# Optimization experiments

Hardware: AMD Instinct MI355X
Metric: run time of the kernel (lower is better)

Reference implementation:

```python
import jax, jax.numpy as jnp
import numpy as np

B = 256        # trees per batch
DEPTH = 10     # complete binary tree depth -> 2^10 - 1 = 1023 internal nodes
N = 2**DEPTH - 1
IN = 128       # input_size
H = 128        # hidden_size
C = 5          # num_classes


def setup_inputs() -> dict:
    key = jax.random.key(0)
    ks = jax.random.split(key, 13)
    gdim = IN + 2 * H  # concat(x, h_left, h_right)
    inp = {"x": jax.random.normal(ks[0], (B, N, IN), jnp.float32)}
    names = ["i", "fl", "fr", "o", "u"]
    for j, nm in enumerate(names):
        inp[f"W_{nm}"] = 0.05 * jax.random.normal(ks[1 + 2 * j], (H, gdim), jnp.float32)
        inp[f"b_{nm}"] = 0.05 * jax.random.normal(ks[2 + 2 * j], (H,), jnp.float32)
    inp["W_cls"] = 0.05 * jax.random.normal(ks[11], (C, H), jnp.float32)
    inp["b_cls"] = 0.05 * jax.random.normal(ks[12], (C,), jnp.float32)
    return inp


def reference(x, W_i, b_i, W_fl, b_fl, W_fr, b_fr, W_o, b_o, W_u, b_u, W_cls, b_cls):
    # Level-order complete binary tree: node k has children 2k+1, 2k+2.
    # Bottom-up sweep; below the deepest internal level all children are
    # empty nodes with h = c = 0 (matches the original base case).
    Bb = x.shape[0]
    h = jnp.zeros((Bb, 2 ** DEPTH, H), x.dtype)
    c = jnp.zeros_like(h)
    for d in range(DEPTH - 1, -1, -1):  # fixed, small structural loop
        n = 2 ** d
        start = n - 1  # level-order offset of level d
        xs = x[:, start:start + n]            # [B, n, IN]
        hl, hr = h[:, 0::2], h[:, 1::2]       # children of node j are 2j, 2j+1 (level-local)
        cl, cr = c[:, 0::2], c[:, 1::2]
        comb = jnp.concatenate([xs, hl, hr], axis=-1)  # [B, n, IN+2H]
        lin = lambda W, b: jnp.einsum('bng,og->bno', comb, W) + b
        i = jax.nn.sigmoid(lin(W_i, b_i))
        fl = jax.nn.sigmoid(lin(W_fl, b_fl))
        fr = jax.nn.sigmoid(lin(W_fr, b_fr))
        o = jax.nn.sigmoid(lin(W_o, b_o))
        u = jnp.tanh(lin(W_u, b_u))
        c = i * u + fl * cl + fr * cr
        h = o * jnp.tanh(c)
    root_h = h[:, 0]                          # [B, H]
    logits = root_h @ W_cls.T + b_cls         # [B, C]
    return logits
```

## Files before the change

### kernel.cpp

```cpp
#include <hip/hip_runtime.h>
#include <hip/hip_bf16.h>
#include <stdint.h>


#define BATCH 256
#define NTOT 1023
#define HDIM 128
#define NCLS 5
#define GDIM 384

typedef __bf16 bf16x8 __attribute__((ext_vector_type(8)));
typedef float f32x4 __attribute__((ext_vector_type(4)));

__device__ __forceinline__ float sigmoid_f(float v) { return 1.f / (1.f + __expf(-v)); }
__device__ __forceinline__ float tanh_f(float v) { return 1.f - 2.f / (1.f + __expf(2.f * v)); }

__global__ __launch_bounds__(256) void pack_w(
    const float* __restrict__ W0, const float* __restrict__ W1, const float* __restrict__ W2,
    const float* __restrict__ W3, const float* __restrict__ W4, __bf16* __restrict__ PW)
{
  int t = blockIdx.x * 256 + threadIdx.x;
  int lane = t & 63;
  int chunk = t >> 6;
  int ks = chunk % 12;
  int jf = (chunk / 12) & 7;
  int g = chunk / 96;
  const float* W = (g == 0) ? W0 : (g == 1) ? W1 : (g == 2) ? W2 : (g == 3) ? W3 : W4;
  const float* s = W + (size_t)(jf * 16 + (lane & 15)) * GDIM + ks * 32 + (lane >> 4) * 8;
  float4 v0 = *(const float4*)s;
  float4 v1 = *(const float4*)(s + 4);
  bf16x8 w;
  w[0] = (__bf16)v0.x; w[1] = (__bf16)v0.y; w[2] = (__bf16)v0.z; w[3] = (__bf16)v0.w;
  w[4] = (__bf16)v1.x; w[5] = (__bf16)v1.y; w[6] = (__bf16)v1.z; w[7] = (__bf16)v1.w;
  *(bf16x8*)(PW + (size_t)t * 8) = w;
}

#define LDS_TOT 75264
#define Q_OFF   50176
#define CSTR    132

template<int NMF, bool LEAF, bool LAST>
__device__ __forceinline__ void fused_level(
    const float* __restrict__ xp,
    const __bf16* __restrict__ PW,
    const float* __restrict__ bv0, const float* __restrict__ bv1,
    const float* __restrict__ bv2, const float* __restrict__ bv3,
    const float* __restrict__ bv4,
    const unsigned char* prev_h, const float* prev_c,
    unsigned char* cur_h, float* cur_c,
    __bf16* __restrict__ gh, float* __restrict__ gc,
    int nvalid)
{
  const int tid = threadIdx.x;
  const int w = tid >> 6;
  const int l = tid & 63;
  const int l15 = l & 15;
  const int quad = l >> 4;
  const int q8 = quad * 8;
  constexpr int NACC = LEAF ? 3 : 5;
  constexpr int NKT = LEAF ? 4 : 12;

  const bf16x8* PB = (const bf16x8*)PW;

  bf16x8 bb[2][NACC];
  bf16x8 xb[2][NMF];

  auto loadB = [&](int buf, int ks) {
#pragma unroll
    for (int q = 0; q < NACC; ++q) {
      const int g = LEAF ? (q ? q + 2 : 0) : q;
      bb[buf][q] = PB[((size_t)(g * 8 + w) * 12 + ks) * 64 + l];
    }
  };
  auto loadX = [&](int buf, int kx) {
#pragma unroll
    for (int mf = 0; mf < NMF; ++mf) {
      const float* xr = xp + (size_t)(mf * 16 + l15) * HDIM + q8 + kx * 32;
      float4 v0 = *(const float4*)xr;
      float4 v1 = *(const float4*)(xr + 4);
      bf16x8 t;
      t[0] = (__bf16)v0.x; t[1] = (__bf16)v0.y; t[2] = (__bf16)v0.z; t[3] = (__bf16)v0.w;
      t[4] = (__bf16)v1.x; t[5] = (__bf16)v1.y; t[6] = (__bf16)v1.z; t[7] = (__bf16)v1.w;
      xb[buf][mf] = t;
    }
  };

  loadB(0, 0);
  loadX(0, 0);
  loadB(1, 1);
  loadX(1, 1);

  f32x4 acc[NMF][NACC];
#pragma unroll
  for (int mf = 0; mf < NMF; ++mf)
#pragma unroll
    for (int q = 0; q < NACC; ++q)
      acc[mf][q] = (f32x4){0.f, 0.f, 0.f, 0.f};

#pragma unroll
  for (int ks = 0; ks < NKT; ++ks) {
    const int cb = ks & 1;
    bf16x8 a[NMF];
#pragma unroll
    for (int mf = 0; mf < NMF; ++mf) {
      if (LEAF || ks < 4) {
        a[mf] = xb[cb][mf];
      } else {
        const int o = (ks < 8) ? 0 : 1;
        const int col2 = ((ks - (o ? 8 : 4)) * 32 + q8) * 2;
        const int nn = 2 * (mf * 16 + l15) + o;
        a[mf] = *(const bf16x8*)(prev_h + nn * 256 + (col2 ^ ((nn & 7) << 4)));
      }
    }
#pragma unroll
    for (int q = 0; q < NACC; ++q)
#pragma unroll
      for (int mf = 0; mf < NMF; ++mf)
        acc[mf][q] = __builtin_amdgcn_mfma_f32_16x16x32_bf16(a[mf], bb[cb][q], acc[mf][q], 0, 0, 0);
    if (ks + 2 < NKT) loadB(cb, ks + 2);
    if (ks + 2 < 4)   loadX(cb, ks + 2);
  }

  const int je = w * 16 + l15;
  const float b0 = bv0[je], b3v = bv3[je], b4v = bv4[je];
#pragma unroll
  for (int mf = 0; mf < NMF; ++mf) {
#pragma unroll
    for (int r = 0; r < 4; ++r) {
      const int me = mf * 16 + quad * 4 + r;
      if (me < nvalid) {
        float gi = sigmoid_f(acc[mf][0][r] + b0);
        float go = sigmoid_f(acc[mf][LEAF ? 1 : 3][r] + b3v);
        float gu = tanh_f(acc[mf][LEAF ? 2 : 4][r] + b4v);
        float cv = gi * gu;
        if constexpr (!LEAF) {
          float gl = sigmoid_f(acc[mf][1][r] + bv1[je]);
          float gr = sigmoid_f(acc[mf][2][r] + bv2[je]);
          cv += gl * prev_c[(2 * me) * CSTR + je] + gr * prev_c[(2 * me + 1) * CSTR + je];
        }
        float hv = go * tanh_f(cv);
        if constexpr (LAST) {
          gc[(size_t)me * HDIM + je] = cv;
          gh[(size_t)me * HDIM + je] = (__bf16)hv;
        } else {
          cur_c[me * CSTR + je] = cv;
          *(__bf16*)(cur_h + me * 256 + ((je * 2) ^ ((me & 7) << 4))) = (__bf16)hv;
        }
      }
    }
  }
}

__global__ __launch_bounds__(512, 4) void fused_top(
    const float* __restrict__ x, const __bf16* __restrict__ PW,
    const float* __restrict__ bv0, const float* __restrict__ bv1,
    const float* __restrict__ bv2, const float* __restrict__ bv3,
    const float* __restrict__ bv4,
    __bf16* __restrict__ h6, float* __restrict__ c6)
{
  __shared__ unsigned char lds[LDS_TOT];
  const int b = blockIdx.x >> 3;
  const int s = blockIdx.x & 7;
  unsigned char* Ph = lds;
  float* Pc = (float*)(lds + 16384);
  unsigned char* Qh = lds + Q_OFF;
  float* Qc = (float*)(lds + Q_OFF + 8192);
  const size_t xb = (size_t)b * NTOT;

  fused_level<4, true, false>(x + (xb + 511 + s * 64) * HDIM, PW,
      bv0, bv1, bv2, bv3, bv4, nullptr, nullptr, Ph, Pc, nullptr, nullptr, 64);
  __syncthreads();
  fused_level<2, false, false>(x + (xb + 255 + s * 32) * HDIM, PW,
      bv0, bv1, bv2, bv3, bv4, Ph, Pc, Qh, Qc, nullptr, nullptr, 32);
  __syncthreads();
  fused_level<1, false, false>(x + (xb + 127 + s * 16) * HDIM, PW,
      bv0, bv1, bv2, bv3, bv4, Qh, Qc, Ph, Pc, nullptr, nullptr, 16);
  __syncthreads();
  fused_level<1, false, true>(x + (xb + 63 + s * 8) * HDIM, PW,
      bv0, bv1, bv2, bv3, bv4, Ph, Pc, nullptr, nullptr,
      h6 + ((size_t)b * 64 + s * 8) * HDIM, c6 + ((size_t)b * 64 + s * 8) * HDIM, 8);
}

__global__ __launch_bounds__(512, 4) void tail_kernel(
    const float* __restrict__ x, const __bf16* __restrict__ PW,
    const float* __restrict__ bv0, const float* __restrict__ bv1,
    const float* __restrict__ bv2, const float* __restrict__ bv3,
    const float* __restrict__ bv4,
    const float* __restrict__ Wcls, const float* __restrict__ bcls,
    const __bf16* __restrict__ h6, const float* __restrict__ c6,
    float* __restrict__ out)
{
  __shared__ unsigned char lds[LDS_TOT];
  const int b = blockIdx.x;
  const int tid = threadIdx.x;
  unsigned char* Ph = lds;
  float* Pc = (float*)(lds + 16384);
  unsigned char* Qh = lds + Q_OFF;
  float* Qc = (float*)(lds + Q_OFF + 8192);

  {
    const __bf16* hs = h6 + (size_t)b * 64 * HDIM;
#pragma unroll
    for (int it = 0; it < 2; ++it) {
      int idx = it * 512 + tid;
      int node = idx >> 4, i8 = idx & 15;
      bf16x8 v = *(const bf16x8*)(hs + node * HDIM + i8 * 8);
      *(bf16x8*)(Ph + node * 256 + ((i8 * 16) ^ ((node & 7) << 4))) = v;
    }
    const float* cs = c6 + (size_t)b * 64 * HDIM;
#pragma unroll
    for (int it = 0; it < 4; ++it) {
      int idx = it * 512 + tid;
      int node = idx >> 5, seg = idx & 31;
      float4 v = *(const float4*)(cs + node * HDIM + seg * 4);
      *(float4*)(Pc + node * CSTR + seg * 4) = v;
    }
  }
  __syncthreads();

  const size_t xb = (size_t)b * NTOT;
  fused_level<2, false, false>(x + (xb + 31) * HDIM, PW,
      bv0, bv1, bv2, bv3, bv4, Ph, Pc, Qh, Qc, nullptr, nullptr, 32);
  __syncthreads();
  fused_level<1, false, false>(x + (xb + 15) * HDIM, PW,
      bv0, bv1, bv2, bv3, bv4, Qh, Qc, Ph, Pc, nullptr, nullptr, 16);
  __syncthreads();
  fused_level<1, false, false>(x + (xb + 7) * HDIM, PW,
      bv0, bv1, bv2, bv3, bv4, Ph, Pc, Qh, Qc, nullptr, nullptr, 8);
  __syncthreads();
  fused_level<1, false, false>(x + (xb + 3) * HDIM, PW,
      bv0, bv1, bv2, bv3, bv4, Qh, Qc, Ph, Pc, nullptr, nullptr, 4);
  __syncthreads();
  fused_level<1, false, false>(x + (xb + 1) * HDIM, PW,
      bv0, bv1, bv2, bv3, bv4, Ph, Pc, Qh, Qc, nullptr, nullptr, 2);
  __syncthreads();
  fused_level<1, false, false>(x + (xb + 0) * HDIM, PW,
      bv0, bv1, bv2, bv3, bv4, Qh, Qc, Ph, Pc, nullptr, nullptr, 1);
  __syncthreads();

  if (tid < NCLS) {
    float sacc = bcls[tid];
    for (int k = 0; k < HDIM; ++k)
      sacc += (float)(*(const __bf16*)(Ph + k * 2)) * Wcls[tid * HDIM + k];
    out[(size_t)b * NCLS + tid] = sacc;
  }
}

extern "C" void kernel_launch(void* const* d_in, const int* in_sizes, int n_in,
                              void* d_out, int out_size, void* d_ws, size_t ws_size,
                              hipStream_t stream) {
  const float* x  = (const float*)d_in[0];
  const float* W[5]  = {(const float*)d_in[1], (const float*)d_in[3], (const float*)d_in[5],
                        (const float*)d_in[7], (const float*)d_in[9]};
  const float* bv[5] = {(const float*)d_in[2], (const float*)d_in[4], (const float*)d_in[6],
                        (const float*)d_in[8], (const float*)d_in[10]};
  const float* Wcls = (const float*)d_in[11];
  const float* bcls = (const float*)d_in[12];

  uint8_t* ws = (uint8_t*)d_ws;
  __bf16* hb1 = (__bf16*)(ws + 33554432);
  float*  cb1 = (float*)(ws + 117440512);
  __bf16* PW  = (__bf16*)(ws + 150994944);

  pack_w<<<120, 256, 0, stream>>>(W[0], W[1], W[2], W[3], W[4], PW);

  fused_top<<<BATCH * 8, 512, 0, stream>>>(
      x, PW, bv[0], bv[1], bv[2], bv[3], bv[4], hb1, cb1);

  tail_kernel<<<BATCH, 512, 0, stream>>>(
      x, PW, bv[0], bv[1], bv[2], bv[3], bv[4],
      Wcls, bcls, hb1, cb1, (float*)d_out);
}
```

Baseline: 544.6 us.

## Drop register double-buffering in fused_level and split leaf level into two halves

```diff
diff --git a/kernel.cpp b/kernel.cpp
--- a/kernel.cpp
+++ b/kernel.cpp
@@ -59,66 +59,62 @@
   const int q8 = quad * 8;
   constexpr int NACC = LEAF ? 3 : 5;
   constexpr int NKT = LEAF ? 4 : 12;
-
   const bf16x8* PB = (const bf16x8*)PW;
 
-  bf16x8 bb[2][NACC];
-  bf16x8 xb[2][NMF];
-
-  auto loadB = [&](int buf, int ks) {
+  f32x4 acc[NMF][NACC];
+#pragma unroll
+  for (int mf = 0; mf < NMF; ++mf)
+#pragma unroll
+    for (int q = 0; q < NACC; ++q)
+      acc[mf][q] = (f32x4){0.f, 0.f, 0.f, 0.f};
+
+#pragma unroll
+  for (int ks = 0; ks < NKT; ++ks) {
+    bf16x8 bq[NACC];
 #pragma unroll
     for (int q = 0; q < NACC; ++q) {
       const int g = LEAF ? (q ? q + 2 : 0) : q;
-      bb[buf][q] = PB[((size_t)(g * 8 + w) * 12 + ks) * 64 + l];
-    }
-  };
-  auto loadX = [&](int buf, int kx) {
-#pragma unroll
-    for (int mf = 0; mf < NMF; ++mf) {
-      const float* xr = xp + (size_t)(mf * 16 + l15) * HDIM + q8 + kx * 32;
-      float4 v0 = *(const float4*)xr;
-      float4 v1 = *(const float4*)(xr + 4);
-      bf16x8 t;
-      t[0] = (__bf16)v0.x; t[1] = (__bf16)v0.y; t[2] = (__bf16)v0.z; t[3] = (__bf16)v0.w;
-      t[4] = (__bf16)v1.x; t[5] = (__bf16)v1.y; t[6] = (__bf16)v1.z; t[7] = (__bf16)v1.w;
-      xb[buf][mf] = t;
-    }
-  };
-
-  loadB(0, 0);
-  loadX(0, 0);
-  loadB(1, 1);
-  loadX(1, 1);
-
-  f32x4 acc[NMF][NACC];
-#pragma unroll
-  for (int mf = 0; mf < NMF; ++mf)
-#pragma unroll
-    for (int q = 0; q < NACC; ++q)
-      acc[mf][q] = (f32x4){0.f, 0.f, 0.f, 0.f};
-
-#pragma unroll
-  for (int ks = 0; ks < NKT; ++ks) {
-    const int cb = ks & 1;
-    bf16x8 a[NMF];
-#pragma unroll
-    for (int mf = 0; mf < NMF; ++mf) {
-      if (LEAF || ks < 4) {
-        a[mf] = xb[cb][mf];
-      } else {
-        const int o = (ks < 8) ? 0 : 1;
-        const int col2 = ((ks - (o ? 8 : 4)) * 32 + q8) * 2;
-        const int nn = 2 * (mf * 16 + l15) + o;
-        a[mf] = *(const bf16x8*)(prev_h + nn * 256 + (col2 ^ ((nn & 7) << 4)));
-      }
-    }
-#pragma unroll
-    for (int q = 0; q < NACC; ++q)
-#pragma unroll
-      for (int mf = 0; mf < NMF; ++mf)
-        acc[mf][q] = __builtin_amdgcn_mfma_f32_16x16x32_bf16(a[mf], bb[cb][q], acc[mf][q], 0, 0, 0);
-    if (ks + 2 < NKT) loadB(cb, ks + 2);
-    if (ks + 2 < 4)   loadX(cb, ks + 2);
+      bq[q] = PB[((size_t)(g * 8 + w) * 12 + ks) * 64 + l];
+    }
+    bf16x8 a0, a1;
+    if (LEAF || ks < 4) {
+      const int kx = LEAF ? ks : ks;
+      {
+        const float* xr = xp + (size_t)l15 * HDIM + q8 + kx * 32;
+        float4 v0 = *(const float4*)xr;
+        float4 v1 = *(const float4*)(xr + 4);
+        bf16x8 t;
+        t[0] = (__bf16)v0.x; t[1] = (__bf16)v0.y; t[2] = (__bf16)v0.z; t[3] = (__bf16)v0.w;
+        t[4] = (__bf16)v1.x; t[5] = (__bf16)v1.y; t[6] = (__bf16)v1.z; t[7] = (__bf16)v1.w;
+        a0 = t;
+      }
+      if constexpr (NMF == 2) {
+        const float* xr = xp + (size_t)(16 + l15) * HDIM + q8 + kx * 32;
+        float4 v0 = *(const float4*)xr;
+        float4 v1 = *(const float4*)(xr + 4);
+        bf16x8 t;
+        t[0] = (__bf16)v0.x; t[1] = (__bf16)v0.y; t[2] = (__bf16)v0.z; t[3] = (__bf16)v0.w;
+        t[4] = (__bf16)v1.x; t[5] = (__bf16)v1.y; t[6] = (__bf16)v1.z; t[7] = (__bf16)v1.w;
+        a1 = t;
+      }
+    } else {
+      const int o = (ks < 8) ? 0 : 1;
+      const int col2 = ((ks - (o ? 8 : 4)) * 32 + q8) * 2;
+      {
+        const int nn = 2 * l15 + o;
+        a0 = *(const bf16x8*)(prev_h + nn * 256 + (col2 ^ ((nn & 7) << 4)));
+      }
+      if constexpr (NMF == 2) {
+        const int nn = 2 * (16 + l15) + o;
+        a1 = *(const bf16x8*)(prev_h + nn * 256 + (col2 ^ ((nn & 7) << 4)));
+      }
+    }
+#pragma unroll
+    for (int q = 0; q < NACC; ++q) {
+      acc[0][q] = __builtin_amdgcn_mfma_f32_16x16x32_bf16(a0, bq[q], acc[0][q], 0, 0, 0);
+      if constexpr (NMF == 2)
+        acc[1][q] = __builtin_amdgcn_mfma_f32_16x16x32_bf16(a1, bq[q], acc[1][q], 0, 0, 0);
+    }
   }
 
   const int je = w * 16 + l15;
@@ -167,8 +163,11 @@
   float* Qc = (float*)(lds + Q_OFF + 8192);
   const size_t xb = (size_t)b * NTOT;
 
-  fused_level<4, true, false>(x + (xb + 511 + s * 64) * HDIM, PW,
-      bv0, bv1, bv2, bv3, bv4, nullptr, nullptr, Ph, Pc, nullptr, nullptr, 64);
+  fused_level<2, true, false>(x + (xb + 511 + s * 64) * HDIM, PW,
+      bv0, bv1, bv2, bv3, bv4, nullptr, nullptr, Ph, Pc, nullptr, nullptr, 32);
+  fused_level<2, true, false>(x + (xb + 511 + s * 64 + 32) * HDIM, PW,
+      bv0, bv1, bv2, bv3, bv4, nullptr, nullptr,
+      Ph + 32 * 256, Pc + 32 * CSTR, nullptr, nullptr, 32);
   __syncthreads();
   fused_level<2, false, false>(x + (xb + 255 + s * 32) * HDIM, PW,
       bv0, bv1, bv2, bv3, bv4, Ph, Pc, Qh, Qc, nullptr, nullptr, 32);
```

Measured after the change: 575.2 us. 1.06x slower.
